# Kernel tuning notes

Measured on AMD Instinct MI355X. Metric: run time of the kernel, lower is better.

The kernel has to match this reference:

```python
import jax, jax.numpy as jnp
import numpy as np

N_DEPTH = 4
N_STACKS = 2
INPUT_SIZE = 1024
HIDDEN_SIZE = 4096
HU = HIDDEN_SIZE // (N_DEPTH * N_STACKS)  # unit_hidden_size = 512
BATCH = 4096


def setup_inputs() -> dict:
    key = jax.random.key(0)
    ks = jax.random.split(key, 8)
    inp = {
        "input": jax.random.normal(ks[0], (BATCH, INPUT_SIZE), dtype=jnp.float32),
        "state": jax.random.normal(ks[1], (2, N_STACKS, BATCH, HIDDEN_SIZE), dtype=jnp.float32),
        # LSTMCell params; residualStack=True -> every cell input dim = INPUT_SIZE
        "W_ih": jax.random.normal(ks[2], (N_DEPTH, N_STACKS, 4 * HU, INPUT_SIZE), dtype=jnp.float32) * 0.05,
        "W_hh": jax.random.normal(ks[3], (N_DEPTH, N_STACKS, 4 * HU, HU), dtype=jnp.float32) * 0.05,
        "b_ih": jax.random.normal(ks[4], (N_DEPTH, N_STACKS, 4 * HU), dtype=jnp.float32) * 0.05,
        "b_hh": jax.random.normal(ks[5], (N_DEPTH, N_STACKS, 4 * HU), dtype=jnp.float32) * 0.05,
        # stacks_proj: Linear(HU, INPUT_SIZE)
        "proj_W": jax.random.normal(ks[6], (INPUT_SIZE, HU), dtype=jnp.float32) * 0.05,
        "proj_b": jax.random.normal(ks[7], (INPUT_SIZE,), dtype=jnp.float32) * 0.05,
    }
    return inp


def _lstm_cell(x, hx, cx, w_ih, w_hh, b_ih, b_hh):
    # gates: [B, 4*HU], PyTorch LSTMCell gate order: i, f, g, o
    gates = x @ w_ih.T + b_ih + hx @ w_hh.T + b_hh
    i_g, f_g, g_g, o_g = jnp.split(gates, 4, axis=-1)
    i_g = jax.nn.sigmoid(i_g)
    f_g = jax.nn.sigmoid(f_g)
    g_g = jnp.tanh(g_g)
    o_g = jax.nn.sigmoid(o_g)
    c_out = f_g * cx + i_g * g_g
    h_out = o_g * jnp.tanh(c_out)
    return h_out, c_out


def reference(input, state, W_ih, W_hh, b_ih, b_hh, proj_W, proj_b):
    # residual=True, residualStack=True
    h_depth, c_depth = [], []
    for i in range(N_DEPTH):
        s, e = i * HU, (i + 1) * HU
        hs, cs = [], []
        dec_input = input
        h_out = None
        for j in range(N_STACKS):
            if j > 0:
                # residualStack: dec_input = dec_input + stacks_proj(h_out)
                dec_input = dec_input + h_out @ proj_W.T + proj_b
            hx = state[0, j, :, s:e]
            cx = state[1, j, :, s:e]
            h_out, c_out = _lstm_cell(dec_input, hx, cx,
                                      W_ih[i, j], W_hh[i, j], b_ih[i, j], b_hh[i, j])
            hs.append(h_out + hx)  # residual=True
            cs.append(c_out)
        h_depth.append(jnp.stack(hs, 0))  # [nStacks, B, HU]
        c_depth.append(jnp.stack(cs, 0))
    # hidden dim is laid out by depth slice: newState[..., i*HU:(i+1)*HU]
    newH = jnp.concatenate(h_depth, axis=-1)  # [nStacks, B, hidden_size]
    newC = jnp.concatenate(c_depth, axis=-1)
    newState = jnp.stack([newH, newC], axis=0)  # [2, nStacks, B, hidden_size]
    ho = newState[0, -1]  # [B, hidden_size]
    return ho, newState
```

## Files before the change

### kernel.cpp

```cpp
#include <hip/hip_runtime.h>
#include <cstdint>
#include <cstddef>

#define B_   4096
#define ISZ  1024
#define SW   4096
#define OHW  2048
#define HU_  512
#define NG   2048

typedef float f32x4 __attribute__((ext_vector_type(4)));
typedef short bf16x8 __attribute__((ext_vector_type(8)));

__device__ __forceinline__ short f2bf(float x) {
    union { float f; unsigned u; } v; v.f = x;
    unsigned r = v.u + 0x7fffu + ((v.u >> 16) & 1u);
    return (short)(r >> 16);
}
__device__ __forceinline__ float sigm(float x)   { return 1.f / (1.f + __expf(-x)); }
__device__ __forceinline__ float tanh_f(float x) { return 2.f / (1.f + __expf(-2.f * x)) - 1.f; }

__device__ __forceinline__ void async16(const void* g, void* l) {
    __builtin_amdgcn_global_load_lds((__attribute__((address_space(1))) void*)g,
                                     (__attribute__((address_space(3))) void*)l,
                                     16, 0, 0);
}

#define VM_BAR(N) asm volatile("s_waitcnt vmcnt(" #N ")\n\ts_barrier" ::: "memory")

__global__ __launch_bounds__(256) void cvt_kernel(const float* __restrict__ src,
                                                  short* __restrict__ dst, long n) {
    long i = ((long)blockIdx.x * 256 + threadIdx.x) * 8;
    if (i >= n) return;
    float4 a = *(const float4*)(src + i);
    float4 b = *(const float4*)(src + i + 4);
    bf16x8 o;
    o[0] = f2bf(a.x); o[1] = f2bf(a.y); o[2] = f2bf(a.z); o[3] = f2bf(a.w);
    o[4] = f2bf(b.x); o[5] = f2bf(b.y); o[6] = f2bf(b.z); o[7] = f2bf(b.w);
    *(bf16x8*)(dst + i) = o;
}

__global__ __launch_bounds__(256) void cvt_h_kernel(const float* __restrict__ src,
                                                    short* __restrict__ dst) {
    long i = ((long)blockIdx.x * 256 + threadIdx.x) * 8;
    long row = i >> 11;
    long c   = i & 2047;
    const float* s = src + row * SW + c;
    float4 a = *(const float4*)(s);
    float4 b = *(const float4*)(s + 4);
    bf16x8 o;
    o[0] = f2bf(a.x); o[1] = f2bf(a.y); o[2] = f2bf(a.z); o[3] = f2bf(a.w);
    o[4] = f2bf(b.x); o[5] = f2bf(b.y); o[6] = f2bf(b.z); o[7] = f2bf(b.w);
    *(bf16x8*)(dst + i) = o;
}

#define MMA_BLK(BB, AR0, N0)                                                      \
  do {                                                                            \
    __builtin_amdgcn_s_setprio(1);                                                \
    _Pragma("unroll")                                                             \
    for (int mtl = 0; mtl < 4; ++mtl) {                                           \
      _Pragma("unroll")                                                           \
      for (int nn = 0; nn < 2; ++nn) {                                            \
        _Pragma("unroll")                                                         \
        for (int ks = 0; ks < 2; ++ks) {                                          \
          acc[(AR0) + mtl][(N0) + nn] = __builtin_amdgcn_mfma_f32_16x16x32_bf16(  \
              aR[mtl][ks], BB[nn][ks], acc[(AR0) + mtl][(N0) + nn], 0, 0, 0);     \
        }                                                                         \
      }                                                                           \
    }                                                                             \
    __builtin_amdgcn_s_setprio(0);                                                \
  } while (0)

#define GROW(rb) (((((rb) >> 4) & 3) << 9) + h0 + ((((rb) >> 6)) << 4) + ((rb) & 15))

__global__ __launch_bounds__(512, 2) void gates2_kernel(
    const short* __restrict__ A1, long a1_dstride,
    const short* __restrict__ Hb,
    const short* __restrict__ Wihb, const short* __restrict__ Whhb,
    const float* __restrict__ b_ih, const float* __restrict__ b_hh,
    const float* __restrict__ state,
    float* __restrict__ out_ho, float* __restrict__ out_state,
    short* __restrict__ h0b,
    int j)
{
    extern __shared__ short lds[];

    const int tid  = threadIdx.x;
    const int wave = tid >> 6;
    const int lane = tid & 63;
    const int wm   = wave >> 2;
    const int wn   = wave & 3;
    const int ln16 = lane & 15;
    const int q    = (lane >> 4) & 3;

    const int id  = blockIdx.x;
    const int swz = (id & 7) * 64 + (id >> 3);
    const int M0  = (swz & 15) * 256;
    const int h0  = ((swz >> 4) & 7) * 64;
    const int d   = swz >> 7;
    const int s   = d * HU_;

    const short* A1d = A1 + (size_t)d * a1_dstride;
    const short* A2  = Hb + (size_t)j * B_ * OHW + s;
    const short* W1  = Wihb + (size_t)(d * 2 + j) * NG * ISZ;
    const short* W2  = Whhb + (size_t)(d * 2 + j) * NG * HU_;
    const float* bi_ = b_ih + (size_t)(d * 2 + j) * NG;
    const float* bh_ = b_hh + (size_t)(d * 2 + j) * NG;

    const int srow = tid >> 3;
    const int scol = (((tid & 7) ^ ((tid >> 3) & 7)) << 3);

    const short* As = A1d;
    const short* Bs = W1;
    unsigned aoff0 = (unsigned)((M0 +   0 + srow) * ISZ + scol);
    unsigned aoff1 = (unsigned)((M0 +  64 + srow) * ISZ + scol);
    unsigned aoff2 = (unsigned)((M0 + 128 + srow) * ISZ + scol);
    unsigned aoff3 = (unsigned)((M0 + 192 + srow) * ISZ + scol);
    unsigned boff0 = (unsigned)(GROW(      srow) * ISZ + scol);
    unsigned boff1 = (unsigned)(GROW( 64 + srow) * ISZ + scol);
    unsigned boff2 = (unsigned)(GROW(128 + srow) * ISZ + scol);
    unsigned boff3 = (unsigned)(GROW(192 + srow) * ISZ + scol);

    const int swz0 = ((q    ) ^ (ln16 & 7)) << 4;
    const int swz1 = ((q + 4) ^ (ln16 & 7)) << 4;
    const char* ldsb = (const char*)lds;

    f32x4 acc[8][4];
#pragma unroll
    for (int i = 0; i < 8; ++i)
#pragma unroll
        for (int n = 0; n < 4; ++n) acc[i][n] = (f32x4){0.f, 0.f, 0.f, 0.f};

    bf16x8 aR[4][2];
    bf16x8 b01[2][2];
    bf16x8 b23[2][2];

    auto stA = [&](unsigned off, int it, int nbuf, int kofs) {
        async16(As + off + kofs, lds + nbuf * 32768 + (it * 64 + wave * 8) * 64);
    };
    auto stB = [&](unsigned off, int it, int nbuf, int kofs) {
        async16(Bs + off + kofs, lds + nbuf * 32768 + 16384 + (it * 64 + wave * 8) * 64);
    };
    auto rdA = [&](int buf, int hi) {
#pragma unroll
        for (int mtl = 0; mtl < 4; ++mtl) {
            const int row = wm * 128 + hi * 64 + mtl * 16 + ln16;
            aR[mtl][0] = *(const bf16x8*)(ldsb + buf * 65536 + row * 128 + swz0);
            aR[mtl][1] = *(const bf16x8*)(ldsb + buf * 65536 + row * 128 + swz1);
        }
    };
    auto rdB = [&](bf16x8 (&bb)[2][2], int buf, int nt0) {
#pragma unroll
        for (int nn = 0; nn < 2; ++nn) {
            const int row = wn * 64 + (nt0 + nn) * 16 + ln16;
            bb[nn][0] = *(const bf16x8*)(ldsb + buf * 65536 + 32768 + row * 128 + swz0);
            bb[nn][1] = *(const bf16x8*)(ldsb + buf * 65536 + 32768 + row * 128 + swz1);
        }
    };

    stB(boff0, 0, 0, 0); stB(boff1, 1, 0, 0); stB(boff2, 2, 0, 0); stB(boff3, 3, 0, 0);
    stA(aoff0, 0, 0, 0); stA(aoff1, 1, 0, 0); stA(aoff2, 2, 0, 0); stA(aoff3, 3, 0, 0);
    VM_BAR(0);

    auto do_tile = [&](int t, int kofs, bool stage) {
        const int buf = t & 1, nbuf = buf ^ 1;
        rdA(buf, 0); rdB(b01, buf, 0);
        if (stage) {
            stB(boff0, 0, nbuf, kofs); stB(boff1, 1, nbuf, kofs);
            stB(boff2, 2, nbuf, kofs); stB(boff3, 3, nbuf, kofs);
            stA(aoff0, 0, nbuf, kofs); stA(aoff1, 1, nbuf, kofs);
            stA(aoff2, 2, nbuf, kofs); stA(aoff3, 3, nbuf, kofs);
        }
        MMA_BLK(b01, 0, 0);
        rdB(b23, buf, 2);
        MMA_BLK(b23, 0, 2);
        rdA(buf, 1);
        MMA_BLK(b23, 4, 2);
        MMA_BLK(b01, 4, 0);
        VM_BAR(0);
    };

    for (int t = 0; t < 15; ++t) do_tile(t, (t + 1) * 64, true);

    As = A2; Bs = W2;
    aoff0 = (unsigned)((M0 +   0 + srow) * OHW + scol);
    aoff1 = (unsigned)((M0 +  64 + srow) * OHW + scol);
    aoff2 = (unsigned)((M0 + 128 + srow) * OHW + scol);
    aoff3 = (unsigned)((M0 + 192 + srow) * OHW + scol);
    boff0 = (unsigned)(GROW(      srow) * HU_ + scol);
    boff1 = (unsigned)(GROW( 64 + srow) * HU_ + scol);
    boff2 = (unsigned)(GROW(128 + srow) * HU_ + scol);
    boff3 = (unsigned)(GROW(192 + srow) * HU_ + scol);

    for (int t = 15; t < 23; ++t) do_tile(t, (t - 15) * 64, true);

    do_tile(23, 0, false);

    const int h   = h0 + wn * 16 + ln16;
    const int col = s + h;
    const float b_i = bi_[h]          + bh_[h];
    const float b_f = bi_[512 + h]    + bh_[512 + h];
    const float b_g = bi_[1024 + h]   + bh_[1024 + h];
    const float b_o = bi_[1536 + h]   + bh_[1536 + h];
#pragma unroll
    for (int mt = 0; mt < 8; ++mt) {
#pragma unroll
        for (int r = 0; r < 4; ++r) {
            const int m = M0 + wm * 128 + mt * 16 + q * 4 + r;
            const float hx = state[((size_t)(j)     * B_ + m) * SW + col];
            const float cx = state[((size_t)(2 + j) * B_ + m) * SW + col];
            const float gi = sigm(acc[mt][0][r] + b_i);
            const float gf = sigm(acc[mt][1][r] + b_f);
            const float gg = tanh_f(acc[mt][2][r] + b_g);
            const float go = sigm(acc[mt][3][r] + b_o);
            const float c_out = gf * cx + gi * gg;
            const float h_out = go * tanh_f(c_out);
            out_state[((size_t)(j)     * B_ + m) * OHW + col] = h_out + hx;
            out_state[((size_t)(2 + j) * B_ + m) * OHW + col] = c_out;
            if (j == 1) out_ho[(size_t)m * OHW + col] = h_out + hx;
            else        h0b[((size_t)d * B_ + m) * HU_ + h] = f2bf(h_out);
        }
    }
}

__global__ __launch_bounds__(256) void proj_kernel(
    const short* __restrict__ h0b, const short* __restrict__ PWb,
    const float* __restrict__ input, const float* __restrict__ proj_b,
    short* __restrict__ dec1b)
{
    __shared__ __align__(16) short sA[128 * 64];
    __shared__ __align__(16) short sB[128 * 64];

    const int t    = threadIdx.x;
    const int wave = t >> 6, lane = t & 63;
    const int ln16 = lane & 15, q = lane >> 4;
    const int d  = blockIdx.z;
    const int M0 = blockIdx.x * 128;
    const int N0 = blockIdx.y * 128;

    const short* A = h0b + (size_t)d * B_ * HU_;

    const int srow = wave * 8 + (lane >> 3);
    const int scol = (((lane & 7) ^ (lane >> 3)) << 3);

    f32x4 acc[2][8];
#pragma unroll
    for (int mt = 0; mt < 2; mt++)
#pragma unroll
        for (int nt = 0; nt < 8; nt++) acc[mt][nt] = (f32x4){0.f, 0.f, 0.f, 0.f};

    for (int k0 = 0; k0 < HU_; k0 += 64) {
#pragma unroll
        for (int it = 0; it < 4; it++)
            async16(A + (size_t)(M0 + it * 32 + srow) * HU_ + k0 + scol,
                    &sA[(it * 32 + wave * 8) * 64]);
#pragma unroll
        for (int it = 0; it < 4; it++)
            async16(PWb + (size_t)(N0 + it * 32 + srow) * HU_ + k0 + scol,
                    &sB[(it * 32 + wave * 8) * 64]);
        __syncthreads();
#pragma unroll
        for (int ks = 0; ks < 2; ks++) {
            const int kb = ks * 4 + q;
            bf16x8 a[2], b[8];
#pragma unroll
            for (int mt = 0; mt < 2; mt++) {
                const int m = wave * 32 + mt * 16 + ln16;
                a[mt] = *(const bf16x8*)&sA[m * 64 + ((kb ^ (m & 7)) << 3)];
            }
#pragma unroll
            for (int nt = 0; nt < 8; nt++) {
                const int n = nt * 16 + ln16;
                b[nt] = *(const bf16x8*)&sB[n * 64 + ((kb ^ (n & 7)) << 3)];
            }
#pragma unroll
            for (int mt = 0; mt < 2; mt++)
#pragma unroll
                for (int nt = 0; nt < 8; nt++)
                    acc[mt][nt] = __builtin_amdgcn_mfma_f32_16x16x32_bf16(a[mt], b[nt], acc[mt][nt], 0, 0, 0);
        }
        __syncthreads();
    }

#pragma unroll
    for (int mt = 0; mt < 2; mt++) {
#pragma unroll
        for (int nt = 0; nt < 8; nt++) {
            const int n = N0 + nt * 16 + ln16;
            const float pb = proj_b[n];
#pragma unroll
            for (int r = 0; r < 4; r++) {
                const int m = M0 + wave * 32 + mt * 16 + q * 4 + r;
                const float y = acc[mt][nt][r] + input[(size_t)m * ISZ + n] + pb;
                dec1b[((size_t)d * B_ + m) * ISZ + n] = f2bf(y);
            }
        }
    }
}

extern "C" void kernel_launch(void* const* d_in, const int* in_sizes, int n_in,
                              void* d_out, int out_size, void* d_ws, size_t ws_size,
                              hipStream_t stream)
{
    const float* input  = (const float*)d_in[0];
    const float* state  = (const float*)d_in[1];
    const float* W_ih   = (const float*)d_in[2];
    const float* W_hh   = (const float*)d_in[3];
    const float* b_ih   = (const float*)d_in[4];
    const float* b_hh   = (const float*)d_in[5];
    const float* proj_W = (const float*)d_in[6];
    const float* proj_b = (const float*)d_in[7];

    float* out_ho    = (float*)d_out;
    float* out_state = out_ho + (size_t)B_ * OHW;

    short* ws    = (short*)d_ws;
    short* Wihb  = ws;
    short* Whhb  = Wihb + (size_t)8 * NG * ISZ;
    short* PWb   = Whhb + (size_t)8 * NG * HU_;
    short* Hb    = PWb  + (size_t)ISZ * HU_;
    short* h0b   = Hb   + (size_t)2 * B_ * OHW;
    short* dec1b = h0b  + (size_t)4 * B_ * HU_;
    short* Xb    = dec1b;

    static bool s_attr = false;
    if (!s_attr) {
        (void)hipFuncSetAttribute(reinterpret_cast<const void*>(gates2_kernel),
                                  hipFuncAttributeMaxDynamicSharedMemorySize, 131072);
        s_attr = true;
    }

    {
        long n;
        n = (long)8 * NG * ISZ;  cvt_kernel<<<dim3((unsigned)(n / 8 / 256)), 256, 0, stream>>>(W_ih,   Wihb, n);
        n = (long)8 * NG * HU_;  cvt_kernel<<<dim3((unsigned)(n / 8 / 256)), 256, 0, stream>>>(W_hh,   Whhb, n);
        n = (long)ISZ * HU_;     cvt_kernel<<<dim3((unsigned)(n / 8 / 256)), 256, 0, stream>>>(proj_W, PWb,  n);
        n = (long)B_ * ISZ;      cvt_kernel<<<dim3((unsigned)(n / 8 / 256)), 256, 0, stream>>>(input,  Xb,   n);
        n = (long)2 * B_ * OHW;  cvt_h_kernel<<<dim3((unsigned)(n / 8 / 256)), 256, 0, stream>>>(state, Hb);
    }

    gates2_kernel<<<dim3(512), dim3(512), 131072, stream>>>(Xb, 0L, Hb, Wihb, Whhb,
                                                            b_ih, b_hh, state,
                                                            out_ho, out_state, h0b, 0);
    proj_kernel<<<dim3(32, 8, 4), 256, 0, stream>>>(h0b, PWb, input, proj_b, dec1b);
    gates2_kernel<<<dim3(512), dim3(512), 131072, stream>>>(dec1b, (long)B_ * ISZ, Hb, Wihb, Whhb,
                                                            b_ih, b_hh, state,
                                                            out_ho, out_state, nullptr, 1);
}
```

Baseline: 728.5 us.

## Load A operand directly from global into registers, stage only B in LDS

```diff
diff --git a/kernel.cpp b/kernel.cpp
--- a/kernel.cpp
+++ b/kernel.cpp
@@ -54,7 +54,7 @@
     *(bf16x8*)(dst + i) = o;
 }
 
-#define MMA_BLK(BB, AR0, N0)                                                      \
+#define MMA_BLK(BB, AA, AR0, N0)                                                  \
   do {                                                                            \
     __builtin_amdgcn_s_setprio(1);                                                \
     _Pragma("unroll")                                                             \
@@ -64,7 +64,7 @@
         _Pragma("unroll")                                                         \
         for (int ks = 0; ks < 2; ++ks) {                                          \
           acc[(AR0) + mtl][(N0) + nn] = __builtin_amdgcn_mfma_f32_16x16x32_bf16(  \
-              aR[mtl][ks], BB[nn][ks], acc[(AR0) + mtl][(N0) + nn], 0, 0, 0);     \
+              AA[mtl][ks], BB[nn][ks], acc[(AR0) + mtl][(N0) + nn], 0, 0, 0);     \
         }                                                                         \
       }                                                                           \
     }                                                                             \
@@ -110,91 +110,93 @@
     const int srow = tid >> 3;
     const int scol = (((tid & 7) ^ ((tid >> 3) & 7)) << 3);
 
-    const short* As = A1d;
-    const short* Bs = W1;
-    unsigned aoff0 = (unsigned)((M0 +   0 + srow) * ISZ + scol);
-    unsigned aoff1 = (unsigned)((M0 +  64 + srow) * ISZ + scol);
-    unsigned aoff2 = (unsigned)((M0 + 128 + srow) * ISZ + scol);
-    unsigned aoff3 = (unsigned)((M0 + 192 + srow) * ISZ + scol);
-    unsigned boff0 = (unsigned)(GROW(      srow) * ISZ + scol);
-    unsigned boff1 = (unsigned)(GROW( 64 + srow) * ISZ + scol);
-    unsigned boff2 = (unsigned)(GROW(128 + srow) * ISZ + scol);
-    unsigned boff3 = (unsigned)(GROW(192 + srow) * ISZ + scol);
+    unsigned b1off[4], b2off[4];
+#pragma unroll
+    for (int it = 0; it < 4; ++it) {
+        const int gr = GROW(it * 64 + srow);
+        b1off[it] = (unsigned)(gr * ISZ + scol);
+        b2off[it] = (unsigned)(gr * HU_ + scol);
+    }
 
     const int swz0 = ((q    ) ^ (ln16 & 7)) << 4;
     const int swz1 = ((q + 4) ^ (ln16 & 7)) << 4;
     const char* ldsb = (const char*)lds;
 
+    const int arow = M0 + wm * 128 + ln16;
+    const int acol = q * 8;
+
     f32x4 acc[8][4];
 #pragma unroll
     for (int i = 0; i < 8; ++i)
 #pragma unroll
         for (int n = 0; n < 4; ++n) acc[i][n] = (f32x4){0.f, 0.f, 0.f, 0.f};
 
-    bf16x8 aR[4][2];
+    bf16x8 aLo[4][2], aHi[4][2];
     bf16x8 b01[2][2];
     bf16x8 b23[2][2];
 
-    auto stA = [&](unsigned off, int it, int nbuf, int kofs) {
-        async16(As + off + kofs, lds + nbuf * 32768 + (it * 64 + wave * 8) * 64);
+    auto ldA = [&](bf16x8 (&ar)[4][2], const short* SA, int strideA, int k0, int hi) {
+#pragma unroll
+        for (int mtl = 0; mtl < 4; ++mtl) {
+            const short* p = SA + (size_t)(arow + hi * 64 + mtl * 16) * strideA + k0 + acol;
+            ar[mtl][0] = *(const bf16x8*)(p);
+            ar[mtl][1] = *(const bf16x8*)(p + 32);
+        }
     };
-    auto stB = [&](unsigned off, int it, int nbuf, int kofs) {
-        async16(Bs + off + kofs, lds + nbuf * 32768 + 16384 + (it * 64 + wave * 8) * 64);
-    };
-    auto rdA = [&](int buf, int hi) {
-#pragma unroll
-        for (int mtl = 0; mtl < 4; ++mtl) {
-            const int row = wm * 128 + hi * 64 + mtl * 16 + ln16;
-            aR[mtl][0] = *(const bf16x8*)(ldsb + buf * 65536 + row * 128 + swz0);
-            aR[mtl][1] = *(const bf16x8*)(ldsb + buf * 65536 + row * 128 + swz1);
-        }
+    auto stB = [&](const short* Bsrc, const unsigned* boff, int nbuf, int kofs) {
+#pragma unroll
+        for (int it = 0; it < 4; ++it)
+            async16(Bsrc + boff[it] + kofs, lds + nbuf * 16384 + (it * 64 + wave * 8) * 64);
     };
     auto rdB = [&](bf16x8 (&bb)[2][2], int buf, int nt0) {
 #pragma unroll
         for (int nn = 0; nn < 2; ++nn) {
             const int row = wn * 64 + (nt0 + nn) * 16 + ln16;
-            bb[nn][0] = *(const bf16x8*)(ldsb + buf * 65536 + 32768 + row * 128 + swz0);
-            bb[nn][1] = *(const bf16x8*)(ldsb + buf * 65536 + 32768 + row * 128 + swz1);
+            bb[nn][0] = *(const bf16x8*)(ldsb + buf * 32768 + row * 128 + swz0);
+            bb[nn][1] = *(const bf16x8*)(ldsb + buf * 32768 + row * 128 + swz1);
         }
     };
 
-    stB(boff0, 0, 0, 0); stB(boff1, 1, 0, 0); stB(boff2, 2, 0, 0); stB(boff3, 3, 0, 0);
-    stA(aoff0, 0, 0, 0); stA(aoff1, 1, 0, 0); stA(aoff2, 2, 0, 0); stA(aoff3, 3, 0, 0);
+    stB(W1, b1off, 0, 0);
+    ldA(aLo, A1d, ISZ, 0, 0);
     VM_BAR(0);
 
-    auto do_tile = [&](int t, int kofs, bool stage) {
+    for (int t = 0; t < 15; ++t) {
         const int buf = t & 1, nbuf = buf ^ 1;
-        rdA(buf, 0); rdB(b01, buf, 0);
-        if (stage) {
-            stB(boff0, 0, nbuf, kofs); stB(boff1, 1, nbuf, kofs);
-            stB(boff2, 2, nbuf, kofs); stB(boff3, 3, nbuf, kofs);
-            stA(aoff0, 0, nbuf, kofs); stA(aoff1, 1, nbuf, kofs);
-            stA(aoff2, 2, nbuf, kofs); stA(aoff3, 3, nbuf, kofs);
-        }
-        MMA_BLK(b01, 0, 0);
-        rdB(b23, buf, 2);
-        MMA_BLK(b23, 0, 2);
-        rdA(buf, 1);
-        MMA_BLK(b23, 4, 2);
-        MMA_BLK(b01, 4, 0);
+        rdB(b01, buf, 0); rdB(b23, buf, 2);
+        MMA_BLK(b01, aLo, 0, 0); MMA_BLK(b23, aLo, 0, 2);
+        ldA(aHi, A1d, ISZ, t * 64, 1);
+        stB(W1, b1off, nbuf, (t + 1) * 64);
+        MMA_BLK(b23, aHi, 4, 2); MMA_BLK(b01, aHi, 4, 0);
+        ldA(aLo, A1d, ISZ, (t + 1) * 64, 0);
         VM_BAR(0);
-    };
-
-    for (int t = 0; t < 15; ++t) do_tile(t, (t + 1) * 64, true);
-
-    As = A2; Bs = W2;
-    aoff0 = (unsigned)((M0 +   0 + srow) * OHW + scol);
-    aoff1 = (unsigned)((M0 +  64 + srow) * OHW + scol);
-    aoff2 = (unsigned)((M0 + 128 + srow) * OHW + scol);
-    aoff3 = (unsigned)((M0 + 192 + srow) * OHW + scol);
-    boff0 = (unsigned)(GROW(      srow) * HU_ + scol);
-    boff1 = (unsigned)(GROW( 64 + srow) * HU_ + scol);
-    boff2 = (unsigned)(GROW(128 + srow) * HU_ + scol);
-    boff3 = (unsigned)(GROW(192 + srow) * HU_ + scol);
-
-    for (int t = 15; t < 23; ++t) do_tile(t, (t - 15) * 64, true);
-
-    do_tile(23, 0, false);
+    }
+    {
+        rdB(b01, 1, 0); rdB(b23, 1, 2);
+        MMA_BLK(b01, aLo, 0, 0); MMA_BLK(b23, aLo, 0, 2);
+        ldA(aHi, A1d, ISZ, 960, 1);
+        stB(W2, b2off, 0, 0);
+        MMA_BLK(b23, aHi, 4, 2); MMA_BLK(b01, aHi, 4, 0);
+        ldA(aLo, A2, OHW, 0, 0);
+        VM_BAR(0);
+    }
+    for (int t = 16; t < 23; ++t) {
+        const int buf = t & 1, nbuf = buf ^ 1;
+        const int k0c = (t - 16) * 64;
+        rdB(b01, buf, 0); rdB(b23, buf, 2);
+        MMA_BLK(b01, aLo, 0, 0); MMA_BLK(b23, aLo, 0, 2);
+        ldA(aHi, A2, OHW, k0c, 1);
+        stB(W2, b2off, nbuf, k0c + 64);
+        MMA_BLK(b23, aHi, 4, 2); MMA_BLK(b01, aHi, 4, 0);
+        ldA(aLo, A2, OHW, k0c + 64, 0);
+        VM_BAR(0);
+    }
+    {
+        rdB(b01, 1, 0); rdB(b23, 1, 2);
+        MMA_BLK(b01, aLo, 0, 0); MMA_BLK(b23, aLo, 0, 2);
+        ldA(aHi, A2, OHW, 448, 1);
+        MMA_BLK(b23, aHi, 4, 2); MMA_BLK(b01, aHi, 4, 0);
+    }
 
     const int h   = h0 + wn * 16 + ln16;
     const int col = s + h;
@@ -326,7 +328,7 @@
     static bool s_attr = false;
     if (!s_attr) {
         (void)hipFuncSetAttribute(reinterpret_cast<const void*>(gates2_kernel),
-                                  hipFuncAttributeMaxDynamicSharedMemorySize, 131072);
+                                  hipFuncAttributeMaxDynamicSharedMemorySize, 65536);
         s_attr = true;
     }
 
@@ -339,11 +341,11 @@
         n = (long)2 * B_ * OHW;  cvt_h_kernel<<<dim3((unsigned)(n / 8 / 256)), 256, 0, stream>>>(state, Hb);
     }
 
-    gates2_kernel<<<dim3(512), dim3(512), 131072, stream>>>(Xb, 0L, Hb, Wihb, Whhb,
-                                                            b_ih, b_hh, state,
-                                                            out_ho, out_state, h0b, 0);
+    gates2_kernel<<<dim3(512), dim3(512), 65536, stream>>>(Xb, 0L, Hb, Wihb, Whhb,
+                                                           b_ih, b_hh, state,
+                                                           out_ho, out_state, h0b, 0);
     proj_kernel<<<dim3(32, 8, 4), 256, 0, stream>>>(h0b, PWb, input, proj_b, dec1b);
-    gates2_kernel<<<dim3(512), dim3(512), 131072, stream>>>(dec1b, (long)B_ * ISZ, Hb, Wihb, Whhb,
-                                                            b_ih, b_hh, state,
-                                                            out_ho, out_state, nullptr, 1);
-}
+    gates2_kernel<<<dim3(512), dim3(512), 65536, stream>>>(dec1b, (long)B_ * ISZ, Hb, Wihb, Whhb,
+                                                           b_ih, b_hh, state,
+                                                           out_ho, out_state, nullptr, 1);
+}
```

Result: slower. 992.6 us (+36.2%).
